# Optimization experiments

Measured on AMD Instinct MI355X. Metric: run time of the kernel, lower is better.

The kernel has to match this reference:

```python
import jax, jax.numpy as jnp
import numpy as np

# init kwargs (constants of the module)
SF = 0.05          # quantization scale factor
GROUP_SIZE = 8     # values per group sharing a term budget
NUM_EXPS = 12      # max number of power-of-two terms kept per group
MAXBITS = 8        # bit-width of the quantized integer magnitude


def setup_inputs() -> dict:
    key = jax.random.key(0)
    x = jax.random.normal(key, (4096, 4096), dtype=jnp.float32)
    return {"x": x}


def _radix2_mod_group(x):
    qmax = 2 ** MAXBITS - 1
    # uniform quantization to signed integers
    q = jnp.clip(jnp.round(x / SF), -qmax, qmax).astype(jnp.int32)
    sign = jnp.sign(q)
    mag = jnp.abs(q)
    g = mag.reshape(-1, GROUP_SIZE)                       # [G, gs]
    exps = jnp.arange(MAXBITS, dtype=jnp.int32)           # [B]
    bits = (g[..., None] >> exps) & 1                     # [G, gs, B] radix-2 terms
    # candidate terms: exponent where the bit is set, -1 otherwise
    cand = jnp.where(bits == 1, exps, -1).reshape(-1, GROUP_SIZE * MAXBITS)
    # keep the NUM_EXPS largest-exponent terms in each group (ties -> lowest index)
    _, idx = jax.lax.top_k(cand, NUM_EXPS)                # [G, NUM_EXPS]
    gidx = jnp.arange(cand.shape[0])[:, None]
    keep = jnp.zeros_like(cand).at[gidx, idx].set(1)      # [G, gs*B]
    keep = keep.reshape(-1, GROUP_SIZE, MAXBITS) * bits   # mask out slots with no term
    recon = jnp.sum(keep << exps, axis=-1)                # [G, gs] kept-term magnitude
    recon = recon * sign.reshape(-1, GROUP_SIZE)
    return (recon.astype(x.dtype) * jnp.asarray(SF, x.dtype)).reshape(x.shape)


def reference(x):
    return _radix2_mod_group(x)
```

## Files before the change

### kernel.cpp

```cpp
#include <hip/hip_runtime.h>


constexpr float SF = 0.05f;
constexpr int NUM_EXPS = 12;

__device__ __forceinline__ unsigned long long transpose8x8(unsigned long long x) {
  unsigned long long t;
  t = (x ^ (x >> 7)) & 0x00AA00AA00AA00AAull; x ^= t ^ (t << 7);
  t = (x ^ (x >> 14)) & 0x0000CCCC0000CCCCull; x ^= t ^ (t << 14);
  t = (x ^ (x >> 28)) & 0x00000000F0F0F0F0ull; x ^= t ^ (t << 28);
  return x;
}

__global__ __launch_bounds__(256) void radix2_mod_group_kernel(
    const float4* __restrict__ xv, float4* __restrict__ ov, int ngroups) {
  int g = blockIdx.x * blockDim.x + threadIdx.x;
  if (g >= ngroups) return;

  float4 a = xv[2 * g];
  float4 b = xv[2 * g + 1];
  float v[8] = {a.x, a.y, a.z, a.w, b.x, b.y, b.z, b.w};

  unsigned long long M = 0ull;
#pragma unroll
  for (int i = 0; i < 8; ++i) {
    float r = rintf(v[i] / SF);
    r = fminf(fmaxf(r, -255.0f), 255.0f);
    int qi = (int)r;
    unsigned mi = (unsigned)(qi < 0 ? -qi : qi);
    M |= (unsigned long long)mi << (8 * (7 - i));
  }

  unsigned long long w = transpose8x8(M);

  int P = __popcll(w);
  int j = P > NUM_EXPS ? P - NUM_EXPS : 0;

  unsigned long long xx = w;
  int pos = 0;
  int c;
  c = __popcll(xx & 0xffffffffull);
  { int t = (j >= c); pos += t << 5; j -= t ? c : 0; xx = t ? (xx >> 32) : xx; }
  c = __popc((unsigned)xx & 0xffffu);
  { int t = (j >= c); pos += t << 4; j -= t ? c : 0; xx = t ? (xx >> 16) : xx; }
  c = __popc((unsigned)xx & 0xffu);
  { int t = (j >= c); pos += t << 3; j -= t ? c : 0; xx = t ? (xx >> 8) : xx; }
  c = __popc((unsigned)xx & 0xfu);
  { int t = (j >= c); pos += t << 2; j -= t ? c : 0; xx = t ? (xx >> 4) : xx; }
  c = __popc((unsigned)xx & 0x3u);
  { int t = (j >= c); pos += t << 1; j -= t ? c : 0; xx = t ? (xx >> 2) : xx; }
  c = (int)((unsigned)xx & 1u);
  { int t = (j >= c); pos += t; }

  unsigned long long keep = w & (~0ull << pos);

  unsigned long long Kt = transpose8x8(keep);

  float o[8];
#pragma unroll
  for (int i = 0; i < 8; ++i) {
    unsigned mi = (unsigned)(Kt >> (8 * (7 - i))) & 0xffu;
    o[i] = copysignf((float)mi * SF, v[i]);
  }

  ov[2 * g] = make_float4(o[0], o[1], o[2], o[3]);
  ov[2 * g + 1] = make_float4(o[4], o[5], o[6], o[7]);
}

extern "C" void kernel_launch(void* const* d_in, const int* in_sizes, int n_in,
                              void* d_out, int out_size, void* d_ws, size_t ws_size,
                              hipStream_t stream) {
  const float* x = (const float*)d_in[0];
  float* out = (float*)d_out;
  int n = in_sizes[0];
  int ngroups = n / 8;
  int block = 256;
  int grid = (ngroups + block - 1) / block;
  radix2_mod_group_kernel<<<grid, block, 0, stream>>>(
      (const float4*)x, (float4*)out, ngroups);
}
```

Baseline: 111.9 us.

## Split each group across two lanes with shuffle and use nontemporal vector IO

Each thread now handles four floats instead of eight. The two halves of a group live in adjacent lanes and are combined with a cross-lane shuffle before the bit-transpose and selection. This is meant to give coalesced contiguous 16-byte accesses per lane and more parallelism for a memory-bound kernel. Loads and stores also use nontemporal builtins to avoid cache pollution. The cost is that both lanes redundantly compute the transpose and selection, plus one shuffle.

```diff
diff --git a/kernel.cpp b/kernel.cpp
--- a/kernel.cpp
+++ b/kernel.cpp
@@ -3,6 +3,8 @@
 
 constexpr float SF = 0.05f;
 constexpr int NUM_EXPS = 12;
+
+typedef float vfloat4 __attribute__((ext_vector_type(4)));
 
 __device__ __forceinline__ unsigned long long transpose8x8(unsigned long long x) {
   unsigned long long t;
@@ -13,58 +15,64 @@
 }
 
 __global__ __launch_bounds__(256) void radix2_mod_group_kernel(
-    const float4* __restrict__ xv, float4* __restrict__ ov, int ngroups) {
-  int g = blockIdx.x * blockDim.x + threadIdx.x;
-  if (g >= ngroups) return;
+    const vfloat4* __restrict__ xv, vfloat4* __restrict__ ov, int nvec) {
+  int t = blockIdx.x * blockDim.x + threadIdx.x;
+  if (t >= nvec) return;
 
-  float4 a = xv[2 * g];
-  float4 b = xv[2 * g + 1];
-  float v[8] = {a.x, a.y, a.z, a.w, b.x, b.y, b.z, b.w};
+  vfloat4 a = __builtin_nontemporal_load(&xv[t]);
+  float v[4] = {a.x, a.y, a.z, a.w};
 
-  unsigned long long M = 0ull;
+  unsigned m4 = 0u;
 #pragma unroll
-  for (int i = 0; i < 8; ++i) {
-    float r = rintf(v[i] / SF);
+  for (int j = 0; j < 4; ++j) {
+    float r = rintf(v[j] / SF);
     r = fminf(fmaxf(r, -255.0f), 255.0f);
-    int qi = (int)r;
-    unsigned mi = (unsigned)(qi < 0 ? -qi : qi);
-    M |= (unsigned long long)mi << (8 * (7 - i));
+    int q = (int)r;
+    unsigned mi = (unsigned)(q < 0 ? -q : q);
+    m4 |= mi << (8 * (3 - j));
   }
+
+  unsigned oth = __shfl_xor(m4, 1, 64);
+  bool evn = ((threadIdx.x & 1) == 0);
+  unsigned hi = evn ? m4 : oth;
+  unsigned lo = evn ? oth : m4;
+  unsigned long long M = ((unsigned long long)hi << 32) | (unsigned long long)lo;
 
   unsigned long long w = transpose8x8(M);
 
   int P = __popcll(w);
-  int j = P > NUM_EXPS ? P - NUM_EXPS : 0;
+  int jj = P > NUM_EXPS ? P - NUM_EXPS : 0;
 
   unsigned long long xx = w;
   int pos = 0;
   int c;
   c = __popcll(xx & 0xffffffffull);
-  { int t = (j >= c); pos += t << 5; j -= t ? c : 0; xx = t ? (xx >> 32) : xx; }
+  { int s = (jj >= c); pos += s << 5; jj -= s ? c : 0; xx = s ? (xx >> 32) : xx; }
   c = __popc((unsigned)xx & 0xffffu);
-  { int t = (j >= c); pos += t << 4; j -= t ? c : 0; xx = t ? (xx >> 16) : xx; }
+  { int s = (jj >= c); pos += s << 4; jj -= s ? c : 0; xx = s ? (xx >> 16) : xx; }
   c = __popc((unsigned)xx & 0xffu);
-  { int t = (j >= c); pos += t << 3; j -= t ? c : 0; xx = t ? (xx >> 8) : xx; }
+  { int s = (jj >= c); pos += s << 3; jj -= s ? c : 0; xx = s ? (xx >> 8) : xx; }
   c = __popc((unsigned)xx & 0xfu);
-  { int t = (j >= c); pos += t << 2; j -= t ? c : 0; xx = t ? (xx >> 4) : xx; }
+  { int s = (jj >= c); pos += s << 2; jj -= s ? c : 0; xx = s ? (xx >> 4) : xx; }
   c = __popc((unsigned)xx & 0x3u);
-  { int t = (j >= c); pos += t << 1; j -= t ? c : 0; xx = t ? (xx >> 2) : xx; }
+  { int s = (jj >= c); pos += s << 1; jj -= s ? c : 0; xx = s ? (xx >> 2) : xx; }
   c = (int)((unsigned)xx & 1u);
-  { int t = (j >= c); pos += t; }
+  { int s = (jj >= c); pos += s; }
 
   unsigned long long keep = w & (~0ull << pos);
 
   unsigned long long Kt = transpose8x8(keep);
 
-  float o[8];
+  unsigned Kmine = evn ? (unsigned)(Kt >> 32) : (unsigned)Kt;
+
+  vfloat4 o;
 #pragma unroll
-  for (int i = 0; i < 8; ++i) {
-    unsigned mi = (unsigned)(Kt >> (8 * (7 - i))) & 0xffu;
-    o[i] = copysignf((float)mi * SF, v[i]);
+  for (int j = 0; j < 4; ++j) {
+    unsigned mi = (Kmine >> (8 * (3 - j))) & 0xffu;
+    o[j] = copysignf((float)mi * SF, v[j]);
   }
 
-  ov[2 * g] = make_float4(o[0], o[1], o[2], o[3]);
-  ov[2 * g + 1] = make_float4(o[4], o[5], o[6], o[7]);
+  __builtin_nontemporal_store(o, &ov[t]);
 }
 
 extern "C" void kernel_launch(void* const* d_in, const int* in_sizes, int n_in,
@@ -73,9 +81,9 @@
   const float* x = (const float*)d_in[0];
   float* out = (float*)d_out;
   int n = in_sizes[0];
-  int ngroups = n / 8;
+  int nvec = n / 4;
   int block = 256;
-  int grid = (ngroups + block - 1) / block;
+  int grid = (nvec + block - 1) / block;
   radix2_mod_group_kernel<<<grid, block, 0, stream>>>(
-      (const float4*)x, (float4*)out, ngroups);
+      (const vfloat4*)x, (vfloat4*)out, nvec);
 }
```

Result: slower. 114.8 us (+2.6%).
